# Optimization experiments

Measured on AMD Instinct MI355X. Metric: run time of the kernel, lower is better.

Reference implementation:

```python
import jax, jax.numpy as jnp
import numpy as np


def setup_inputs() -> dict:
    key = jax.random.key(0)
    ks = jax.random.split(key, 4)
    T, B, E = 2048, 2, 1024
    query = jax.random.normal(ks[0], (T, B, E), dtype=jnp.float32)
    attn_mask = jnp.zeros((T, T), dtype=jnp.float32)
    Wqkv = jax.random.normal(ks[1], (3 * E, E), dtype=jnp.float32) * 0.02
    bqkv = jnp.zeros((3 * E,), dtype=jnp.float32)
    Wout = jax.random.normal(ks[2], (E, E), dtype=jnp.float32) * 0.02
    bout = jnp.zeros((E,), dtype=jnp.float32)
    return {"query": query, "attn_mask": attn_mask, "Wqkv": Wqkv,
            "bqkv": bqkv, "Wout": Wout, "bout": bout, "num_heads": 16}


def reference(query, attn_mask, Wqkv, bqkv, Wout, bout, num_heads):
    T, B, E = query.shape
    H = num_heads
    hd = E // H
    scaling = hd ** -0.5
    # fused QKV projection: [T,B,3E]
    qkv = jnp.einsum('tbe,fe->tbf', query, Wqkv) + bqkv
    q, k, v = jnp.split(qkv, 3, axis=-1)
    q = q * scaling
    # [T,B,E] -> [B*H, T, hd]
    def to_heads(x):
        return x.reshape(T, B * H, hd).transpose(1, 0, 2)
    q, k, v = to_heads(q), to_heads(k), to_heads(v)
    # scores [B*H, T, T]
    scores = jnp.einsum('bth,bsh->bts', q, k) + attn_mask[None, :, :]
    probs = jax.nn.softmax(scores, axis=-1)  # dropout p=0
    attn = jnp.einsum('bts,bsh->bth', probs, v)  # [B*H, T, hd]
    attn = attn.transpose(1, 0, 2).reshape(T, B, E)
    out = jnp.einsum('tbe,fe->tbf', attn, Wout) + bout
    avg_w = probs.reshape(B, H, T, T).sum(axis=1) / H
    return out, avg_w
```

## Files before the change

kernel.cpp:

```cpp
#include <hip/hip_runtime.h>
#include <cstdint>
#include <cstddef>

#define Tt 2048
#define Bb 2
#define Ee 1024
#define Hh 16
#define HD 64
#define BHh (Bb*Hh)
#define Mm (Tt*Bb)

typedef short bf16x8 __attribute__((ext_vector_type(8)));
typedef float f32x4  __attribute__((ext_vector_type(4)));

#define MFMA16(a,b,c) __builtin_amdgcn_mfma_f32_16x16x32_bf16(a, b, c, 0, 0, 0)

__device__ __forceinline__ unsigned short f2bf(float f) {
    unsigned int u = __builtin_bit_cast(unsigned int, f);
    u += 0x7FFFu + ((u >> 16) & 1u);
    return (unsigned short)(u >> 16);
}
__device__ __forceinline__ unsigned int pack2bf(float lo, float hi) {
    unsigned int r;
    asm("v_cvt_pk_bf16_f32 %0, %1, %2" : "=v"(r) : "v"(lo), "v"(hi));
    return r;
}

__device__ __forceinline__ int swzA(int row, int dwcol) {
    return (row*32 + dwcol) ^ ((row & 7) << 2);
}
__device__ __forceinline__ int swzG(int row, int dwcol) {
    return (row*16 + dwcol) ^ ((row & 3) << 2);
}

__device__ __forceinline__ bf16x8 ldfrag(const unsigned short* base, int row, int col) {
    const unsigned int* p = (const unsigned int*)(base + row*66 + col);
    const unsigned int* q = (const unsigned int*)(base + row*66 + col + 16);
    uint4 u;
    u.x = p[0]; u.y = p[1];
    u.z = q[0]; u.w = q[1];
    return __builtin_bit_cast(bf16x8, u);
}

__global__ __launch_bounds__(256)
void to_bf16(const float* __restrict__ src, unsigned short* __restrict__ dst, int n8)
{
    const int stride = gridDim.x * 256;
    for (int i = blockIdx.x*256 + threadIdx.x; i < n8; i += stride) {
        const float4 a = ((const float4*)src)[2*i];
        const float4 b = ((const float4*)src)[2*i + 1];
        const uint4 u = {pack2bf(a.x,a.y), pack2bf(a.z,a.w),
                         pack2bf(b.x,b.y), pack2bf(b.z,b.w)};
        ((uint4*)dst)[i] = u;
    }
}

template<int MODE>
__global__ __launch_bounds__(256)
void gemm_mfma(const unsigned short* __restrict__ A, const unsigned short* __restrict__ W,
               const float* __restrict__ bias, float* __restrict__ Cout,
               unsigned short* __restrict__ qbuf, unsigned short* __restrict__ kbuf,
               unsigned short* __restrict__ vbuf, int N, int K)
{
    __shared__ __align__(16) unsigned int AsDW[2][128*16];
    __shared__ __align__(16) unsigned int WsDW[2][128*16];
    const int tid  = threadIdx.x;
    const int bm   = blockIdx.y * 128;
    const int bn   = blockIdx.x * 128;
    const int w    = tid >> 6;
    const int lane = tid & 63;
    const int lr   = lane & 15;
    const int lg   = lane >> 4;
    const int wm   = (w >> 1) * 64;
    const int wn   = (w & 1) * 64;

    f32x4 acc[4][4];
#pragma unroll
    for (int m = 0; m < 4; ++m)
#pragma unroll
        for (int n = 0; n < 4; ++n)
            acc[m][n] = f32x4{0.f, 0.f, 0.f, 0.f};

    const int r1  = tid >> 2;
    const int cdw = (tid & 3) * 4;

    {
        const uint4 a0 = *(const uint4*)&A[(size_t)(bm + r1)      * K + cdw*2];
        const uint4 a1 = *(const uint4*)&A[(size_t)(bm + r1 + 64) * K + cdw*2];
        const uint4 w0 = *(const uint4*)&W[(size_t)(bn + r1)      * K + cdw*2];
        const uint4 w1 = *(const uint4*)&W[(size_t)(bn + r1 + 64) * K + cdw*2];
        *(uint4*)(AsDW[0] + swzG(r1,      cdw)) = a0;
        *(uint4*)(AsDW[0] + swzG(r1 + 64, cdw)) = a1;
        *(uint4*)(WsDW[0] + swzG(r1,      cdw)) = w0;
        *(uint4*)(WsDW[0] + swzG(r1 + 64, cdw)) = w1;
        __syncthreads();
    }

    int cur = 0;
    for (int k0 = 0; k0 < K; k0 += 32) {
        const bool has_next = (k0 + 32 < K);
        uint4 an0, an1, wn0, wn1;
        if (has_next) {
            an0 = *(const uint4*)&A[(size_t)(bm + r1)      * K + k0 + 32 + cdw*2];
            an1 = *(const uint4*)&A[(size_t)(bm + r1 + 64) * K + k0 + 32 + cdw*2];
            wn0 = *(const uint4*)&W[(size_t)(bn + r1)      * K + k0 + 32 + cdw*2];
            wn1 = *(const uint4*)&W[(size_t)(bn + r1 + 64) * K + k0 + 32 + cdw*2];
        }

        const unsigned int* Ac = AsDW[cur];
        const unsigned int* Wc = WsDW[cur];
        bf16x8 af[4], wf[4];
#pragma unroll
        for (int i = 0; i < 4; ++i) {
            af[i] = __builtin_bit_cast(bf16x8, *(const uint4*)(Ac + swzG(wm + 16*i + lr, 4*lg)));
            wf[i] = __builtin_bit_cast(bf16x8, *(const uint4*)(Wc + swzG(wn + 16*i + lr, 4*lg)));
        }
#pragma unroll
        for (int m = 0; m < 4; ++m)
#pragma unroll
            for (int n = 0; n < 4; ++n)
                acc[m][n] = MFMA16(af[m], wf[n], acc[m][n]);

        if (has_next) {
            *(uint4*)(AsDW[cur ^ 1] + swzG(r1,      cdw)) = an0;
            *(uint4*)(AsDW[cur ^ 1] + swzG(r1 + 64, cdw)) = an1;
            *(uint4*)(WsDW[cur ^ 1] + swzG(r1,      cdw)) = wn0;
            *(uint4*)(WsDW[cur ^ 1] + swzG(r1 + 64, cdw)) = wn1;
        }
        __syncthreads();
        cur ^= 1;
    }

#pragma unroll
    for (int nsub = 0; nsub < 4; ++nsub) {
        const int n0 = bn + wn + 16*nsub + lr;
        const float bv = bias[n0];
#pragma unroll
        for (int msub = 0; msub < 4; ++msub) {
#pragma unroll
            for (int reg = 0; reg < 4; ++reg) {
                const int m = bm + wm + 16*msub + 4*lg + reg;
                float v = acc[msub][nsub][reg] + bv;
                if (MODE == 0) {
                    const int which = n0 >> 10;
                    const int e0 = n0 & 1023;
                    const int h = e0 >> 6, d0 = e0 & 63;
                    if (which == 0) v *= 0.125f;
                    unsigned short* dst = (which == 0) ? qbuf : (which == 1) ? kbuf : vbuf;
                    dst[((size_t)((m & 1)*Hh + h) * Tt + (m >> 1)) * HD + d0] = f2bf(v);
                } else {
                    Cout[(size_t)m * N + n0] = v;
                }
            }
        }
    }
}

__global__ __launch_bounds__(512)
void attn_mfma(const unsigned short* __restrict__ qb, const unsigned short* __restrict__ kb,
               const unsigned short* __restrict__ vb, const float* __restrict__ mask,
               unsigned short* __restrict__ attnb, float* __restrict__ lbuf)
{
    __shared__ __align__(16) unsigned int KsDW[2][64*32];
    __shared__ __align__(16) unsigned short Vt[2][64*66];
    __shared__ float l_sh[128];

    const int tid  = threadIdx.x;
    const int bid  = blockIdx.x;
    const int wid  = (bid & 7) * 64 + (bid >> 3);
    const int bh   = wid & 31;
    const int t0   = (wid >> 5) * 128;
    const int w    = tid >> 6;
    const int lane = tid & 63;
    const int lr   = lane & 15;
    const int lg   = lane >> 4;
    const int b = bh >> 4, h = bh & 15;

    const unsigned short* __restrict__ Qg = qb + (size_t)bh * Tt * HD;
    const unsigned short* __restrict__ Kg = kb + (size_t)bh * Tt * HD;
    const unsigned short* __restrict__ Vg = vb + (size_t)bh * Tt * HD;

    const int str = tid >> 3;
    const int sdw = (tid & 7) * 4;

    const int vdg = tid & 15;
    const int vs2 = tid >> 4;

    bf16x8 qf[2];
    for (int half = 0; half < 2; ++half) {
        __syncthreads();
        *(uint4*)(KsDW[0] + swzA(str, sdw)) =
            *(const uint4*)&Qg[(size_t)(t0 + half*64 + str) * HD + sdw*2];
        __syncthreads();
        if ((w >> 2) == half) {
            const int r = 16*(w & 3) + lr;
            qf[0] = __builtin_bit_cast(bf16x8, *(const uint4*)(KsDW[0] + swzA(r, 4*lg)));
            qf[1] = __builtin_bit_cast(bf16x8, *(const uint4*)(KsDW[0] + swzA(r, 16 + 4*lg)));
        }
    }

    f32x4 oacc[4];
#pragma unroll
    for (int d = 0; d < 4; ++d)
        oacc[d] = f32x4{0.f, 0.f, 0.f, 0.f};
    float lacc = 0.f;

    {
        const uint4 k0r = *(const uint4*)&Kg[(size_t)str * HD + sdw*2];
        const uint2 a0  = *(const uint2*)&Vg[(size_t)(2*vs2)     * HD + vdg*4];
        const uint2 c0  = *(const uint2*)&Vg[(size_t)(2*vs2 + 1) * HD + vdg*4];
        __syncthreads();
        *(uint4*)(KsDW[0] + swzA(str, sdw)) = k0r;
        unsigned short* vt0 = &Vt[0][0];
        *(unsigned int*)&vt0[(vdg*4+0)*66 + 2*vs2] = (a0.x & 0xFFFFu) | (c0.x << 16);
        *(unsigned int*)&vt0[(vdg*4+1)*66 + 2*vs2] = (a0.x >> 16)     | (c0.x & 0xFFFF0000u);
        *(unsigned int*)&vt0[(vdg*4+2)*66 + 2*vs2] = (a0.y & 0xFFFFu) | (c0.y << 16);
        *(unsigned int*)&vt0[(vdg*4+3)*66 + 2*vs2] = (a0.y >> 16)     | (c0.y & 0xFFFF0000u);
        __syncthreads();
    }

    int cur = 0;
    for (int s0 = 0; s0 < Tt; s0 += 64) {
        const bool has_next = (s0 + 64 < Tt);
        uint4 kn; uint2 van, vcn;
        if (has_next) {
            kn  = *(const uint4*)&Kg[(size_t)(s0 + 64 + str) * HD + sdw*2];
            van = *(const uint2*)&Vg[(size_t)(s0 + 64 + 2*vs2)     * HD + vdg*4];
            vcn = *(const uint2*)&Vg[(size_t)(s0 + 64 + 2*vs2 + 1) * HD + vdg*4];
        }

        const unsigned int* Kc = KsDW[cur];
        const unsigned short* Vc = &Vt[cur][0];

        f32x4 sacc[4];
#pragma unroll
        for (int ssub = 0; ssub < 4; ++ssub) {
            const bf16x8 a0 = __builtin_bit_cast(bf16x8,
                *(const uint4*)(Kc + swzA(16*ssub + lr, 4*lg)));
            const bf16x8 a1 = __builtin_bit_cast(bf16x8,
                *(const uint4*)(Kc + swzA(16*ssub + lr, 16 + 4*lg)));
            f32x4 z = {0.f, 0.f, 0.f, 0.f};
            z = MFMA16(a0, qf[0], z);
            z = MFMA16(a1, qf[1], z);
            sacc[ssub] = z;
        }

        unsigned int pw[8];
        {
            float lt = 0.f;
            const float* __restrict__ mrow =
                &mask[(size_t)(t0 + 16*w + lr) * Tt + s0];
#pragma unroll
            for (int ssub = 0; ssub < 4; ++ssub) {
                const float4 mv = *(const float4*)&mrow[16*ssub + 4*lg];
                const float e0 = __expf(sacc[ssub][0] + mv.x);
                const float e1 = __expf(sacc[ssub][1] + mv.y);
                const float e2 = __expf(sacc[ssub][2] + mv.z);
                const float e3 = __expf(sacc[ssub][3] + mv.w);
                lt += (e0 + e1) + (e2 + e3);
                pw[ssub*2]     = pack2bf(e0, e1);
                pw[ssub*2 + 1] = pack2bf(e2, e3);
            }
            lt += __shfl_xor(lt, 16);
            lt += __shfl_xor(lt, 32);
            lacc += lt;
        }

        const uint4 ua = {pw[0], pw[1], pw[2], pw[3]};
        const uint4 ub = {pw[4], pw[5], pw[6], pw[7]};
#pragma unroll
        for (int dsub = 0; dsub < 4; ++dsub) {
            const bf16x8 b0 = ldfrag(Vc, 16*dsub + lr, 4*lg);
            const bf16x8 b1 = ldfrag(Vc, 16*dsub + lr, 32 + 4*lg);
            oacc[dsub] = MFMA16(__builtin_bit_cast(bf16x8, ua), b0, oacc[dsub]);
            oacc[dsub] = MFMA16(__builtin_bit_cast(bf16x8, ub), b1, oacc[dsub]);
        }

        if (has_next) {
            *(uint4*)(KsDW[cur ^ 1] + swzA(str, sdw)) = kn;
            unsigned short* vt1 = &Vt[cur ^ 1][0];
            *(unsigned int*)&vt1[(vdg*4+0)*66 + 2*vs2] = (van.x & 0xFFFFu) | (vcn.x << 16);
            *(unsigned int*)&vt1[(vdg*4+1)*66 + 2*vs2] = (van.x >> 16)     | (vcn.x & 0xFFFF0000u);
            *(unsigned int*)&vt1[(vdg*4+2)*66 + 2*vs2] = (van.y & 0xFFFFu) | (vcn.y << 16);
            *(unsigned int*)&vt1[(vdg*4+3)*66 + 2*vs2] = (van.y >> 16)     | (vcn.y & 0xFFFF0000u);
        }
        __syncthreads();
        cur ^= 1;
    }

    if (lg == 0) l_sh[16*w + lr] = lacc;
    __syncthreads();
#pragma unroll
    for (int reg = 0; reg < 4; ++reg) {
        const int tl = 16*w + 4*lg + reg;
        const float inv = 1.f / l_sh[tl];
        const int t = t0 + tl;
#pragma unroll
        for (int dsub = 0; dsub < 4; ++dsub)
            attnb[((size_t)t * Bb + b) * Ee + h*HD + dsub*16 + lr] =
                f2bf(oacc[dsub][reg] * inv);
    }
    if (lg == 0)
        lbuf[(size_t)bh * Tt + t0 + 16*w + lr] = lacc;
}

__global__ __launch_bounds__(256)
void avg_probs_mfma(const unsigned short* __restrict__ qb, const unsigned short* __restrict__ kb,
                    const float* __restrict__ mask, const float* __restrict__ lbuf,
                    float* __restrict__ avg)
{
    __shared__ __align__(16) unsigned short Qs[2][64*66];
    __shared__ __align__(16) unsigned short Ksh[2][64*66];
    __shared__ float linv[16][64];

    const int tid  = threadIdx.x;
    const int b    = blockIdx.z;
    const int t0   = blockIdx.y * 64;
    const int s0   = blockIdx.x * 64;
    const int w    = tid >> 6;
    const int lane = tid & 63;
    const int lr   = lane & 15;
    const int lg   = lane >> 4;

    const int str = tid >> 2;
    const int stc = (tid & 3) * 16;

    {
        const int hh = tid >> 4, tl = (tid & 15) * 4;
        const float4 lv = *(const float4*)&lbuf[(size_t)(b*Hh + hh) * Tt + t0 + tl];
        linv[hh][tl+0] = 1.f / (16.f * lv.x);
        linv[hh][tl+1] = 1.f / (16.f * lv.y);
        linv[hh][tl+2] = 1.f / (16.f * lv.z);
        linv[hh][tl+3] = 1.f / (16.f * lv.w);

        const unsigned short* Qp = &qb[((size_t)(b*Hh) * Tt + t0 + str) * HD + stc];
        const unsigned short* Kp = &kb[((size_t)(b*Hh) * Tt + s0 + str) * HD + stc];
        const uint4 q0 = *(const uint4*)Qp;
        const uint4 q1 = *(const uint4*)(Qp + 8);
        const uint4 k0 = *(const uint4*)Kp;
        const uint4 k1 = *(const uint4*)(Kp + 8);
        *(uint4*)&Qs[0][str*66 + stc]      = q0;
        *(uint4*)&Qs[0][str*66 + stc + 8]  = q1;
        *(uint4*)&Ksh[0][str*66 + stc]     = k0;
        *(uint4*)&Ksh[0][str*66 + stc + 8] = k1;
        __syncthreads();
    }

    f32x4 mf[4];
#pragma unroll
    for (int ssub = 0; ssub < 4; ++ssub)
#pragma unroll
        for (int reg = 0; reg < 4; ++reg)
            mf[ssub][reg] = mask[(size_t)(t0 + 16*w + 4*lg + reg) * Tt + s0 + 16*ssub + lr];

    f32x4 av[4];
#pragma unroll
    for (int ssub = 0; ssub < 4; ++ssub) av[ssub] = f32x4{0.f, 0.f, 0.f, 0.f};

    int cur = 0;
    for (int h = 0; h < Hh; ++h) {
        const bool has_next = (h + 1 < Hh);
        uint4 qn0, qn1, kn0, kn1;
        if (has_next) {
            const unsigned short* Qp = &qb[((size_t)(b*Hh + h + 1) * Tt + t0 + str) * HD + stc];
            const unsigned short* Kp = &kb[((size_t)(b*Hh + h + 1) * Tt + s0 + str) * HD + stc];
            qn0 = *(const uint4*)Qp;
            qn1 = *(const uint4*)(Qp + 8);
            kn0 = *(const uint4*)Kp;
            kn1 = *(const uint4*)(Kp + 8);
        }

        const unsigned short* Qc = &Qs[cur][0];
        const unsigned short* Kc = &Ksh[cur][0];

        const float lv0 = linv[h][16*w + 4*lg + 0];
        const float lv1 = linv[h][16*w + 4*lg + 1];
        const float lv2 = linv[h][16*w + 4*lg + 2];
        const float lv3 = linv[h][16*w + 4*lg + 3];

        const bf16x8 af0 = ldfrag(Qc, 16*w + lr, 4*lg);
        const bf16x8 af1 = ldfrag(Qc, 16*w + lr, 32 + 4*lg);
#pragma unroll
        for (int ssub = 0; ssub < 4; ++ssub) {
            const bf16x8 bf0 = ldfrag(Kc, 16*ssub + lr, 4*lg);
            const bf16x8 bf1 = ldfrag(Kc, 16*ssub + lr, 32 + 4*lg);
            f32x4 z = {0.f, 0.f, 0.f, 0.f};
            z = MFMA16(af0, bf0, z);
            z = MFMA16(af1, bf1, z);
            av[ssub][0] += __expf(z[0] + mf[ssub][0]) * lv0;
            av[ssub][1] += __expf(z[1] + mf[ssub][1]) * lv1;
            av[ssub][2] += __expf(z[2] + mf[ssub][2]) * lv2;
            av[ssub][3] += __expf(z[3] + mf[ssub][3]) * lv3;
        }

        if (has_next) {
            *(uint4*)&Qs[cur ^ 1][str*66 + stc]      = qn0;
            *(uint4*)&Qs[cur ^ 1][str*66 + stc + 8]  = qn1;
            *(uint4*)&Ksh[cur ^ 1][str*66 + stc]     = kn0;
            *(uint4*)&Ksh[cur ^ 1][str*66 + stc + 8] = kn1;
        }
        __syncthreads();
        cur ^= 1;
    }

#pragma unroll
    for (int ssub = 0; ssub < 4; ++ssub)
#pragma unroll
        for (int reg = 0; reg < 4; ++reg)
            avg[((size_t)b * Tt + t0 + 16*w + 4*lg + reg) * Tt + s0 + 16*ssub + lr] =
                av[ssub][reg];
}

extern "C" void kernel_launch(void* const* d_in, const int* in_sizes, int n_in,
                              void* d_out, int out_size, void* d_ws, size_t ws_size,
                              hipStream_t stream)
{
    (void)in_sizes; (void)n_in; (void)out_size; (void)ws_size;
    const float* query = (const float*)d_in[0];
    const float* mask  = (const float*)d_in[1];
    const float* Wqkv  = (const float*)d_in[2];
    const float* bqkv  = (const float*)d_in[3];
    const float* Wout  = (const float*)d_in[4];
    const float* bout  = (const float*)d_in[5];

    float* out = (float*)d_out;
    float* avg = out + (size_t)Tt * Bb * Ee;

    const size_t S1 = (size_t)BHh * Tt * HD;
    unsigned short* wsu     = (unsigned short*)d_ws;
    unsigned short* qbuf    = wsu;
    unsigned short* kbuf    = qbuf + S1;
    unsigned short* vbuf    = kbuf + S1;
    unsigned short* attnb   = vbuf + S1;
    unsigned short* querybf = attnb + (size_t)Mm * Ee;
    unsigned short* wqkvbf  = querybf + (size_t)Mm * Ee;
    unsigned short* woutbf  = wqkvbf + (size_t)3 * Ee * Ee;
    float*          lbuf    = (float*)(woutbf + (size_t)Ee * Ee);

    to_bf16<<<1024, 256, 0, stream>>>(query, querybf, (Mm*Ee)/8);
    to_bf16<<<1024, 256, 0, stream>>>(Wqkv, wqkvbf, (3*Ee*Ee)/8);
    to_bf16<<<512,  256, 0, stream>>>(Wout, woutbf, (Ee*Ee)/8);

    gemm_mfma<0><<<dim3(3072/128, Mm/128), 256, 0, stream>>>(
        querybf, wqkvbf, bqkv, nullptr, qbuf, kbuf, vbuf, 3072, Ee);
    attn_mfma<<<dim3(BHh * (Tt/128)), 512, 0, stream>>>(
        qbuf, kbuf, vbuf, mask, attnb, lbuf);
    avg_probs_mfma<<<dim3(Tt/64, Tt/64, Bb), 256, 0, stream>>>(
        qbuf, kbuf, mask, lbuf, avg);
    gemm_mfma<1><<<dim3(Ee/128, Mm/128), 256, 0, stream>>>(
        attnb, woutbf, bout, out, nullptr, nullptr, nullptr, Ee, Ee);
}
```

Baseline: 198.1 us.

## Write V pre-transposed and permuted from QKV GEMM to simplify attention loads

The QKV projection epilogue now stores V in a per-64-row tile, transposed, column-permuted layout that matches the MFMA B-operand fragment order. The attention kernel can then load V tiles with single 16-byte vector loads into a swizzled LDS buffer, the same way it loads K. This removes the per-tile shuffle and transpose in the attention loop and the padded, conflict-prone LDS reads. In exchange the GEMM epilogue writes V in a scattered pattern, which may cost some store efficiency.

```diff
diff --git a/kernel.cpp b/kernel.cpp
--- a/kernel.cpp
+++ b/kernel.cpp
@@ -145,9 +145,17 @@
                     const int which = n0 >> 10;
                     const int e0 = n0 & 1023;
                     const int h = e0 >> 6, d0 = e0 & 63;
+                    const int t = m >> 1, bb = m & 1;
                     if (which == 0) v *= 0.125f;
-                    unsigned short* dst = (which == 0) ? qbuf : (which == 1) ? kbuf : vbuf;
-                    dst[((size_t)((m & 1)*Hh + h) * Tt + (m >> 1)) * HD + d0] = f2bf(v);
+                    if (which == 2) {
+                        const int tile = t >> 6, sc = t & 63;
+                        const int col = (sc & 3) | (((sc >> 4) & 1) << 2) |
+                                        (((sc >> 2) & 3) << 3) | ((sc >> 5) << 5);
+                        vbuf[(((size_t)(bb*Hh + h) * 32 + tile) * 64 + d0) * 64 + col] = f2bf(v);
+                    } else {
+                        unsigned short* dst = (which == 0) ? qbuf : kbuf;
+                        dst[((size_t)(bb*Hh + h) * Tt + t) * HD + d0] = f2bf(v);
+                    }
                 } else {
                     Cout[(size_t)m * N + n0] = v;
                 }
@@ -162,7 +170,7 @@
                unsigned short* __restrict__ attnb, float* __restrict__ lbuf)
 {
     __shared__ __align__(16) unsigned int KsDW[2][64*32];
-    __shared__ __align__(16) unsigned short Vt[2][64*66];
+    __shared__ __align__(16) unsigned int VtDW[2][64*32];
     __shared__ float l_sh[128];
 
     const int tid  = threadIdx.x;
@@ -183,9 +191,6 @@
     const int str = tid >> 3;
     const int sdw = (tid & 7) * 4;
 
-    const int vdg = tid & 15;
-    const int vs2 = tid >> 4;
-
     bf16x8 qf[2];
     for (int half = 0; half < 2; ++half) {
         __syncthreads();
@@ -207,30 +212,24 @@
 
     {
         const uint4 k0r = *(const uint4*)&Kg[(size_t)str * HD + sdw*2];
-        const uint2 a0  = *(const uint2*)&Vg[(size_t)(2*vs2)     * HD + vdg*4];
-        const uint2 c0  = *(const uint2*)&Vg[(size_t)(2*vs2 + 1) * HD + vdg*4];
+        const uint4 v0r = *(const uint4*)&Vg[(size_t)str * 64 + sdw*2];
         __syncthreads();
         *(uint4*)(KsDW[0] + swzA(str, sdw)) = k0r;
-        unsigned short* vt0 = &Vt[0][0];
-        *(unsigned int*)&vt0[(vdg*4+0)*66 + 2*vs2] = (a0.x & 0xFFFFu) | (c0.x << 16);
-        *(unsigned int*)&vt0[(vdg*4+1)*66 + 2*vs2] = (a0.x >> 16)     | (c0.x & 0xFFFF0000u);
-        *(unsigned int*)&vt0[(vdg*4+2)*66 + 2*vs2] = (a0.y & 0xFFFFu) | (c0.y << 16);
-        *(unsigned int*)&vt0[(vdg*4+3)*66 + 2*vs2] = (a0.y >> 16)     | (c0.y & 0xFFFF0000u);
+        *(uint4*)(VtDW[0] + swzA(str, sdw)) = v0r;
         __syncthreads();
     }
 
     int cur = 0;
     for (int s0 = 0; s0 < Tt; s0 += 64) {
         const bool has_next = (s0 + 64 < Tt);
-        uint4 kn; uint2 van, vcn;
-        if (has_next) {
-            kn  = *(const uint4*)&Kg[(size_t)(s0 + 64 + str) * HD + sdw*2];
-            van = *(const uint2*)&Vg[(size_t)(s0 + 64 + 2*vs2)     * HD + vdg*4];
-            vcn = *(const uint2*)&Vg[(size_t)(s0 + 64 + 2*vs2 + 1) * HD + vdg*4];
+        uint4 kn, vn;
+        if (has_next) {
+            kn = *(const uint4*)&Kg[(size_t)(s0 + 64 + str) * HD + sdw*2];
+            vn = *(const uint4*)&Vg[((size_t)((s0 >> 6) + 1) * 64 + str) * 64 + sdw*2];
         }
 
         const unsigned int* Kc = KsDW[cur];
-        const unsigned short* Vc = &Vt[cur][0];
+        const unsigned int* VcDW = VtDW[cur];
 
         f32x4 sacc[4];
 #pragma unroll
@@ -270,19 +269,17 @@
         const uint4 ub = {pw[4], pw[5], pw[6], pw[7]};
 #pragma unroll
         for (int dsub = 0; dsub < 4; ++dsub) {
-            const bf16x8 b0 = ldfrag(Vc, 16*dsub + lr, 4*lg);
-            const bf16x8 b1 = ldfrag(Vc, 16*dsub + lr, 32 + 4*lg);
+            const bf16x8 b0 = __builtin_bit_cast(bf16x8,
+                *(const uint4*)(VcDW + swzA(16*dsub + lr, 4*lg)));
+            const bf16x8 b1 = __builtin_bit_cast(bf16x8,
+                *(const uint4*)(VcDW + swzA(16*dsub + lr, 16 + 4*lg)));
             oacc[dsub] = MFMA16(__builtin_bit_cast(bf16x8, ua), b0, oacc[dsub]);
             oacc[dsub] = MFMA16(__builtin_bit_cast(bf16x8, ub), b1, oacc[dsub]);
         }
 
         if (has_next) {
             *(uint4*)(KsDW[cur ^ 1] + swzA(str, sdw)) = kn;
-            unsigned short* vt1 = &Vt[cur ^ 1][0];
-            *(unsigned int*)&vt1[(vdg*4+0)*66 + 2*vs2] = (van.x & 0xFFFFu) | (vcn.x << 16);
-            *(unsigned int*)&vt1[(vdg*4+1)*66 + 2*vs2] = (van.x >> 16)     | (vcn.x & 0xFFFF0000u);
-            *(unsigned int*)&vt1[(vdg*4+2)*66 + 2*vs2] = (van.y & 0xFFFFu) | (vcn.y << 16);
-            *(unsigned int*)&vt1[(vdg*4+3)*66 + 2*vs2] = (van.y >> 16)     | (vcn.y & 0xFFFF0000u);
+            *(uint4*)(VtDW[cur ^ 1] + swzA(str, sdw)) = vn;
         }
         __syncthreads();
         cur ^= 1;
```

After: 205.2 us. 3.6% more time.
